# Kernel optimization log

Measured on AMD Instinct MI355X. Metric: run time of the kernel, lower is better.

## Reference

```python
import jax, jax.numpy as jnp
import numpy as np

N = 100000   # nodes
E = 1600000  # edges
D = 64       # input_size == hidden_size
L = 2        # n_layer


def setup_inputs() -> dict:
    key = jax.random.key(0)
    ks = jax.random.split(key, 16)
    s = 1.0 / np.sqrt(D)  # glorot-ish scale
    inp = jax.random.normal(ks[0], (N, D), jnp.float32)
    h = jax.random.normal(ks[1], (L, N, D), jnp.float32)
    edgidx = jax.random.randint(ks[2], (2, E), 0, N, jnp.int32)
    W = lambda i: jax.random.normal(ks[i], (L, D, D), jnp.float32) * s
    b = lambda i: jax.random.normal(ks[i], (L, D), jnp.float32) * 0.01
    return {
        'inp': inp, 'h': h, 'edgidx': edgidx,
        'Wxz': W(3), 'Whz': W(4), 'Wxr': W(5), 'Whr': W(6), 'Wxh': W(7), 'Whh': W(8),
        'bxz': b(9), 'bhz': b(10), 'bxr': b(11), 'bhr': b(12), 'bxh': b(13), 'bhh': b(14),
    }


def _gcn_norm(edgidx):
    # add self loops with weight 2 (improved=True), symmetric deg^-1/2 normalization
    row, col = edgidx[0], edgidx[1]
    loop = jnp.arange(N, dtype=row.dtype)
    row_f = jnp.concatenate([row, loop])
    col_f = jnp.concatenate([col, loop])
    w = jnp.concatenate([jnp.ones((E,), jnp.float32), 2.0 * jnp.ones((N,), jnp.float32)])
    deg = jax.ops.segment_sum(w, row_f, num_segments=N)
    dinv = jnp.where(deg > 0, deg ** -0.5, 0.0)
    norm = dinv[row_f] * w * dinv[col_f]
    return row_f, col_f, norm


def _gcn(x, Wt, bt, row_f, col_f, norm):
    # out[i] = sum_{(j->i)} norm_e * (x @ W)[j] + b   (PyG flow: gather at edge_index[0], scatter at edge_index[1])
    y = x @ Wt
    out = jax.ops.segment_sum(norm[:, None] * y[row_f], col_f, num_segments=N)
    return out + bt


def reference(inp, h, edgidx, Wxz, Whz, Wxr, Whr, Wxh, Whh, bxz, bhz, bxr, bhr, bxh, bhh):
    row_f, col_f, norm = _gcn_norm(edgidx)
    g = lambda x, W, b, i: _gcn(x, W[i], b[i], row_f, col_f, norm)
    x_in = inp
    outs = []
    for i in range(L):
        z = jax.nn.sigmoid(g(x_in, Wxz, bxz, i) + g(h[i], Whz, bhz, i))
        r = jax.nn.sigmoid(g(x_in, Wxr, bxr, i) + g(h[i], Whr, bhr, i))
        h_t = jnp.tanh(g(x_in, Wxh, bxh, i) + g(r * h[i], Whh, bhh, i))
        ho = z * h[i] + (1.0 - z) * h_t
        outs.append(ho)
        x_in = ho
    h_out = jnp.stack(outs)
    return (h_out, h_out)
```

## Files before the change

kernel.cpp:

```cpp
#include <hip/hip_runtime.h>
#include <hip/hip_fp16.h>
#include <math.h>
#include <stdint.h>

#define DD 64
#define CHUNK 1024
#define NRG 512
#define BB  128

using f16x8 = __attribute__((ext_vector_type(8))) _Float16;
using f32x4 = __attribute__((ext_vector_type(4))) float;

static inline int divup(int a, int b){ return (a + b - 1) / b; }

__global__ __launch_bounds__(256) void bin_k(
    const int* __restrict__ edg, int E, int per, int nr, int cap,
    unsigned int* __restrict__ bufc, unsigned short* __restrict__ bufr,
    int* __restrict__ cntc, int* __restrict__ cntr)
{
  extern __shared__ int cur[];
  int* curc = cur;
  int* curr = cur + nr;
  const int b = blockIdx.x, t = threadIdx.x;
  for (int i = t; i < 2 * nr; i += 256) cur[i] = 0;
  __syncthreads();
  const int e0 = b * per;
  const int e1 = (e0 + per < E) ? e0 + per : E;
  unsigned int* mybufc = bufc + (size_t)b * nr * cap;
  unsigned short* mybufr = bufr + (size_t)b * nr * cap;
  for (int e = e0 + t; e < e1; e += 256){
    int r = edg[e];
    int c = edg[E + e];
    int rg = c >> 9;
    int p = atomicAdd(&curc[rg], 1);
    if (p < cap) mybufc[rg * cap + p] = ((unsigned int)r << 9) | (unsigned int)(c & 511);
    int rr = r >> 9;
    int q = atomicAdd(&curr[rr], 1);
    if (q < cap) mybufr[rr * cap + q] = (unsigned short)(r & 511);
  }
  __syncthreads();
  for (int i = t; i < nr; i += 256){
    int vc = curc[i]; cntc[b * nr + i] = vc < cap ? vc : cap;
    int vr = curr[i]; cntr[b * nr + i] = vr < cap ? vr : cap;
  }
}

__global__ __launch_bounds__(256) void cnt2_k(
    const unsigned int* __restrict__ bufc, const unsigned short* __restrict__ bufr,
    const int* __restrict__ cntc, const int* __restrict__ cntr,
    int nb, int nr, int cap,
    int* __restrict__ colcnt, int* __restrict__ rowcnt, int N)
{
  __shared__ int lhc[NRG];
  __shared__ int lhr[NRG];
  __shared__ int lcc[BB];
  __shared__ int lcr[BB];
  const int rg = blockIdx.x, t = threadIdx.x;
  for (int i = t; i < NRG; i += 256){ lhc[i] = 0; lhr[i] = 0; }
  for (int i = t; i < nb; i += 256){ lcc[i] = cntc[i * nr + rg]; lcr[i] = cntr[i * nr + rg]; }
  __syncthreads();
  const int wv = t >> 6, lane = t & 63;
  for (int b = wv; b < nb; b += 4){
    const unsigned int* buf = bufc + ((size_t)b * nr + rg) * cap;
    int cnt = lcc[b];
    for (int i = lane; i < cnt; i += 64) atomicAdd(&lhc[buf[i] & 511], 1);
    const unsigned short* bufR = bufr + ((size_t)b * nr + rg) * cap;
    int cntR = lcr[b];
    for (int i = lane; i < cntR; i += 64) atomicAdd(&lhr[bufR[i]], 1);
  }
  __syncthreads();
  for (int i = t; i < NRG; i += 256){
    int node = rg * NRG + i;
    if (node < N){ colcnt[node] = lhc[i]; rowcnt[node] = lhr[i]; }
  }
}

__global__ void scan1_k(const int* __restrict__ cnt, const int* __restrict__ rowcnt,
                        float* __restrict__ dinv, int* __restrict__ bsum, int N){
  __shared__ int sh[256];
  int t = threadIdx.x;
  int base = blockIdx.x * CHUNK + t * 4;
  int s = 0;
  #pragma unroll
  for (int j = 0; j < 4; j++){
    int g = base + j;
    if (g < N){
      s += cnt[g];
      dinv[g] = 1.0f / sqrtf((float)rowcnt[g] + 2.0f);
    }
  }
  sh[t] = s; __syncthreads();
  for (int off = 128; off > 0; off >>= 1){
    if (t < off) sh[t] += sh[t + off];
    __syncthreads();
  }
  if (t == 0) bsum[blockIdx.x] = sh[0];
}

__global__ void scan2_k(const int* __restrict__ bsum, int* __restrict__ bpre, int NB){
  __shared__ int sh[128];
  int t = threadIdx.x;
  int v = (t < NB) ? bsum[t] : 0;
  sh[t] = v; __syncthreads();
  for (int off = 1; off < 128; off <<= 1){
    int x = (t >= off) ? sh[t - off] : 0;
    __syncthreads();
    sh[t] += x;
    __syncthreads();
  }
  if (t < NB) bpre[t] = sh[t] - v;
}

__global__ void scan3_k(const int* __restrict__ cnt, const int* __restrict__ bpre,
                        int* __restrict__ offsets, int N){
  __shared__ int sh[256];
  int t = threadIdx.x, b = blockIdx.x;
  int base = b * CHUNK + t * 4;
  int v[4]; int s = 0;
  #pragma unroll
  for (int j = 0; j < 4; j++){ int g = base + j; v[j] = (g < N) ? cnt[g] : 0; s += v[j]; }
  sh[t] = s; __syncthreads();
  for (int off = 1; off < 256; off <<= 1){
    int x = (t >= off) ? sh[t - off] : 0;
    __syncthreads();
    sh[t] += x;
    __syncthreads();
  }
  int run = sh[t] - s + bpre[b];
  #pragma unroll
  for (int j = 0; j < 4; j++){
    int g = base + j;
    if (g <= N) offsets[g] = run;
    run += v[j];
  }
}

__global__ __launch_bounds__(256) void scat_k(
    const unsigned int* __restrict__ bufc, const int* __restrict__ cntc,
    int nb, int nr, int cap, const int* __restrict__ offsets,
    const float* __restrict__ dinv,
    int* __restrict__ csr_src, float* __restrict__ csr_w, int N)
{
  __shared__ int loff[NRG];
  __shared__ float ldinv[NRG];
  __shared__ int lcc[BB];
  const int rg = blockIdx.x, t = threadIdx.x;
  for (int i = t; i < NRG; i += 256){
    int node = rg * NRG + i;
    loff[i]  = (node < N) ? offsets[node] : 0;
    ldinv[i] = (node < N) ? dinv[node] : 0.0f;
  }
  for (int i = t; i < nb; i += 256) lcc[i] = cntc[i * nr + rg];
  __syncthreads();
  const int wv = t >> 6, lane = t & 63;
  for (int b = wv; b < nb; b += 4){
    const unsigned int* buf = bufc + ((size_t)b * nr + rg) * cap;
    int cnt = lcc[b];
    for (int i = lane; i < cnt; i += 64){
      unsigned int v = buf[i];
      int lo = v & 511;
      int sn = (int)(v >> 9);
      int p = atomicAdd(&loff[lo], 1);
      csr_src[p] = sn;
      csr_w[p] = dinv[sn] * ldinv[lo];
    }
  }
}

__global__ void pack0_k(const float* __restrict__ X, const float* __restrict__ H,
                        __half2* __restrict__ XH, int total){
  int i = blockIdx.x * 256 + threadIdx.x;
  if (i < total){
    __half2 v;
    v.x = __float2half_rn(X[i]);
    v.y = __float2half_rn(H[i]);
    XH[i] = v;
  }
}

__global__ void packb_k(const float* __restrict__ Wxz, const float* __restrict__ Whz,
                        const float* __restrict__ Wxr, const float* __restrict__ Whr,
                        const float* __restrict__ Wxh, const float* __restrict__ Whh,
                        const float* __restrict__ bxz, const float* __restrict__ bhz,
                        const float* __restrict__ bxr, const float* __restrict__ bhr,
                        const float* __restrict__ bxh, const float* __restrict__ bhh,
                        _Float16* __restrict__ Bg, _Float16* __restrict__ Bo,
                        float* __restrict__ biasg, int L){
  const int PER = 24576 + 4096 + 192;
  int tid = blockIdx.x * 256 + threadIdx.x;
  if (tid >= L * PER) return;
  int l = tid / PER, r = tid % PER;
  if (r < 24576){
    int q = r;
    int s = q & 7, lane = (q >> 3) & 63, ks = (q >> 9) & 3, jt = q >> 11;
    int k = ks * 32 + (lane >> 4) * 8 + s;
    int b = jt >> 2;
    int j = (jt & 3) * 16 + (lane & 15);
    const float* Wx = (b == 0) ? Wxz : (b == 1) ? Wxr : Wxh;
    const float* Wh = (b == 0) ? Whz : Whr;
    float v;
    if (k < 64) v = Wx[(size_t)l * 4096 + k * 64 + j];
    else        v = (b == 2) ? 0.0f : Wh[(size_t)l * 4096 + (k - 64) * 64 + j];
    Bg[(size_t)l * 24576 + q] = (_Float16)v;
  } else if (r < 24576 + 4096){
    int q = r - 24576;
    int s = q & 7, lane = (q >> 3) & 63, ks = (q >> 9) & 1, jt = q >> 10;
    int k = ks * 32 + (lane >> 4) * 8 + s;
    int j = jt * 16 + (lane & 15);
    Bo[(size_t)l * 4096 + q] = (_Float16)Whh[(size_t)l * 4096 + k * 64 + j];
  } else {
    int j = r - (24576 + 4096);
    int b = j >> 6, jj = j & 63;
    float v = (b == 0) ? bxz[l * 64 + jj] + bhz[l * 64 + jj]
            : (b == 1) ? bxr[l * 64 + jj] + bhr[l * 64 + jj]
                       : bxh[l * 64 + jj] + bhh[l * 64 + jj];
    biasg[l * 192 + j] = v;
  }
}

__global__ void agg2_k(const __half2* __restrict__ XH,
                       const int* __restrict__ offsets, const int* __restrict__ src,
                       const float* __restrict__ w, const float* __restrict__ dinv,
                       _Float16* __restrict__ AXAH, int N){
  int wid = (blockIdx.x * blockDim.x + threadIdx.x) >> 6;
  int lane = threadIdx.x & 63;
  if (wid >= N) return;
  float dv = dinv[wid];
  float selfw = 2.0f * dv * dv;
  size_t me = (size_t)wid * DD + lane;
  float2 sf = __half22float2(XH[me]);
  float ax[8], ah[8];
  #pragma unroll
  for (int j = 0; j < 8; j++){ ax[j] = 0.0f; ah[j] = 0.0f; }
  ax[0] = selfw * sf.x; ah[0] = selfw * sf.y;
  int s0 = offsets[wid], s1 = offsets[wid + 1];
  int e = s0;
  for (; e + 8 <= s1; e += 8){
    int   sn[8];
    float wn[8];
    float2 f[8];
    #pragma unroll
    for (int j = 0; j < 8; j++){ sn[j] = src[e + j]; wn[j] = w[e + j]; }
    #pragma unroll
    for (int j = 0; j < 8; j++) f[j] = __half22float2(XH[(size_t)sn[j] * DD + lane]);
    #pragma unroll
    for (int j = 0; j < 8; j++){
      ax[j] += wn[j] * f[j].x;
      ah[j] += wn[j] * f[j].y;
    }
  }
  for (; e < s1; ++e){
    float wa = w[e];
    float2 fa = __half22float2(XH[(size_t)src[e] * DD + lane]);
    ax[0] += wa * fa.x;
    ah[0] += wa * fa.y;
  }
  float axs = ((ax[0] + ax[1]) + (ax[2] + ax[3])) + ((ax[4] + ax[5]) + (ax[6] + ax[7]));
  float ahs = ((ah[0] + ah[1]) + (ah[2] + ah[3])) + ((ah[4] + ah[5]) + (ah[6] + ah[7]));
  size_t o = (size_t)wid * 128 + lane;
  AXAH[o]      = (_Float16)axs;
  AXAH[o + 64] = (_Float16)ahs;
}

__global__ void agg1_k(const _Float16* __restrict__ RH,
                       const int* __restrict__ offsets, const int* __restrict__ src,
                       const float* __restrict__ w, const float* __restrict__ dinv,
                       _Float16* __restrict__ Arh, int N){
  int wid = (blockIdx.x * blockDim.x + threadIdx.x) >> 6;
  int lane = threadIdx.x & 63;
  if (wid >= N) return;
  float dv = dinv[wid];
  float selfw = 2.0f * dv * dv;
  size_t me = (size_t)wid * DD + lane;
  float ax[8];
  #pragma unroll
  for (int j = 0; j < 8; j++) ax[j] = 0.0f;
  ax[0] = selfw * (float)RH[me];
  int s0 = offsets[wid], s1 = offsets[wid + 1];
  int e = s0;
  for (; e + 8 <= s1; e += 8){
    int   sn[8];
    float wn[8];
    float f[8];
    #pragma unroll
    for (int j = 0; j < 8; j++){ sn[j] = src[e + j]; wn[j] = w[e + j]; }
    #pragma unroll
    for (int j = 0; j < 8; j++) f[j] = (float)RH[(size_t)sn[j] * DD + lane];
    #pragma unroll
    for (int j = 0; j < 8; j++) ax[j] += wn[j] * f[j];
  }
  for (; e < s1; ++e){
    ax[0] += w[e] * (float)RH[(size_t)src[e] * DD + lane];
  }
  Arh[me] = (_Float16)(((ax[0] + ax[1]) + (ax[2] + ax[3])) + ((ax[4] + ax[5]) + (ax[6] + ax[7])));
}

__global__ __launch_bounds__(256) void gatem_k(
    const _Float16* __restrict__ AXAH, const float* __restrict__ Hh,
    const _Float16* __restrict__ Bg, const float* __restrict__ biasg,
    _Float16* __restrict__ zb, _Float16* __restrict__ rhb,
    _Float16* __restrict__ t1b, int N)
{
  const int lane = threadIdx.x & 63;
  const int wv   = threadIdx.x >> 6;
  const long nbase = ((long)blockIdx.x * 4 + wv) * 32;
  if (nbase >= N) return;
  const int m  = lane & 15;
  const int kb = lane >> 4;

  f32x4 acc[2][12];
  #pragma unroll
  for (int jt = 0; jt < 12; jt++){
    float bv = biasg[jt * 16 + m];
    f32x4 b4 = {bv, bv, bv, bv};
    acc[0][jt] = b4;
    acc[1][jt] = b4;
  }

  #pragma unroll 1
  for (int ks = 0; ks < 4; ks++){
    f16x8 af0, af1;
    {
      long r0 = nbase + m;           if (r0 >= N) r0 = N - 1;
      long r1 = nbase + 16 + m;      if (r1 >= N) r1 = N - 1;
      af0 = *(const f16x8*)(AXAH + (size_t)r0 * 128 + ks * 32 + kb * 8);
      af1 = *(const f16x8*)(AXAH + (size_t)r1 * 128 + ks * 32 + kb * 8);
    }
    #pragma unroll
    for (int jt = 0; jt < 12; jt++){
      f16x8 bf = *(const f16x8*)(Bg + ((size_t)(jt * 4 + ks) * 64 + lane) * 8);
      acc[0][jt] = __builtin_amdgcn_mfma_f32_16x16x32_f16(af0, bf, acc[0][jt], 0, 0, 0);
      acc[1][jt] = __builtin_amdgcn_mfma_f32_16x16x32_f16(af1, bf, acc[1][jt], 0, 0, 0);
    }
  }

  #pragma unroll
  for (int mt = 0; mt < 2; mt++){
    #pragma unroll
    for (int i = 0; i < 4; i++){
      long row = nbase + mt * 16 + kb * 4 + i;
      if (row < N){
        #pragma unroll
        for (int jq = 0; jq < 4; jq++){
          int j = jq * 16 + m;
          size_t o = (size_t)row * 64 + j;
          float zpre = acc[mt][jq][i];
          float rpre = acc[mt][4 + jq][i];
          float t1v  = acc[mt][8 + jq][i];
          float hv = Hh[o];
          zb[o]  = (_Float16)(1.0f / (1.0f + __expf(-zpre)));
          rhb[o] = (_Float16)(hv / (1.0f + __expf(-rpre)));
          t1b[o] = (_Float16)t1v;
        }
      }
    }
  }
}

__global__ __launch_bounds__(256) void outm_k(
    const _Float16* __restrict__ Arh, const _Float16* __restrict__ t1b,
    const _Float16* __restrict__ zb, const float* __restrict__ Hh,
    const _Float16* __restrict__ Bo,
    float* __restrict__ o1, float* __restrict__ o2,
    const float* __restrict__ hNext, __half2* __restrict__ XHnext,
    int doPack, int N)
{
  const int lane = threadIdx.x & 63;
  const int wv   = threadIdx.x >> 6;
  const long nbase = ((long)blockIdx.x * 4 + wv) * 32;
  if (nbase >= N) return;
  const int m  = lane & 15;
  const int kb = lane >> 4;

  f32x4 acc[2][4];
  #pragma unroll
  for (int mt = 0; mt < 2; mt++){
    #pragma unroll
    for (int jt = 0; jt < 4; jt++){
      #pragma unroll
      for (int i = 0; i < 4; i++){
        long row = nbase + mt * 16 + kb * 4 + i;
        if (row >= N) row = N - 1;
        acc[mt][jt][i] = (float)t1b[(size_t)row * 64 + jt * 16 + m];
      }
    }
  }

  #pragma unroll
  for (int ks = 0; ks < 2; ks++){
    f16x8 af0, af1;
    {
      long r0 = nbase + m;           if (r0 >= N) r0 = N - 1;
      long r1 = nbase + 16 + m;      if (r1 >= N) r1 = N - 1;
      af0 = *(const f16x8*)(Arh + (size_t)r0 * 64 + ks * 32 + kb * 8);
      af1 = *(const f16x8*)(Arh + (size_t)r1 * 64 + ks * 32 + kb * 8);
    }
    #pragma unroll
    for (int jt = 0; jt < 4; jt++){
      f16x8 bf = *(const f16x8*)(Bo + ((size_t)(jt * 2 + ks) * 64 + lane) * 8);
      acc[0][jt] = __builtin_amdgcn_mfma_f32_16x16x32_f16(af0, bf, acc[0][jt], 0, 0, 0);
      acc[1][jt] = __builtin_amdgcn_mfma_f32_16x16x32_f16(af1, bf, acc[1][jt], 0, 0, 0);
    }
  }

  #pragma unroll
  for (int mt = 0; mt < 2; mt++){
    #pragma unroll
    for (int i = 0; i < 4; i++){
      long row = nbase + mt * 16 + kb * 4 + i;
      if (row < N){
        #pragma unroll
        for (int jt = 0; jt < 4; jt++){
          int j = jt * 16 + m;
          size_t o = (size_t)row * 64 + j;
          float e = __expf(2.0f * acc[mt][jt][i]);
          float ht = 1.0f - 2.0f / (e + 1.0f);
          float z = (float)zb[o];
          float hv = Hh[o];
          float ho = z * hv + (1.0f - z) * ht;
          o1[o] = ho;
          o2[o] = ho;
          if (doPack){
            __half2 v;
            v.x = __float2half_rn(ho);
            v.y = __float2half_rn(hNext[o]);
            XHnext[o] = v;
          }
        }
      }
    }
  }
}

extern "C" void kernel_launch(void* const* d_in, const int* in_sizes, int n_in,
                              void* d_out, int out_size, void* d_ws, size_t ws_size,
                              hipStream_t stream){
  const float* inp = (const float*)d_in[0];
  const float* h   = (const float*)d_in[1];
  const int*   edg = (const int*)d_in[2];
  const float* Wxz = (const float*)d_in[3];
  const float* Whz = (const float*)d_in[4];
  const float* Wxr = (const float*)d_in[5];
  const float* Whr = (const float*)d_in[6];
  const float* Wxh = (const float*)d_in[7];
  const float* Whh = (const float*)d_in[8];
  const float* bxz = (const float*)d_in[9];
  const float* bhz = (const float*)d_in[10];
  const float* bxr = (const float*)d_in[11];
  const float* bhr = (const float*)d_in[12];
  const float* bxh = (const float*)d_in[13];
  const float* bhh = (const float*)d_in[14];
  float* out = (float*)d_out;

  const int ND = in_sizes[0];
  const int N  = ND / DD;
  const int E  = in_sizes[2] / 2;
  const int L  = in_sizes[1] / ND;

  const int nr  = divup(N, NRG);
  const int per = divup(E, BB);
  const int cap = (per / nr) * 3 + 64;

  char* p = (char*)d_ws;
  auto alloc = [&](size_t bytes) -> void* {
    void* r = (void*)p;
    p += ((bytes + 255) / 256) * 256;
    return r;
  };
  auto a256 = [](size_t b) -> size_t { return ((b + 255) / 256) * 256; };

  int*      offsets = (int*)alloc((size_t)(N + 1) * 4);
  int*      bsum    = (int*)alloc(128 * 4);
  int*      bpre    = (int*)alloc(128 * 4);
  float*    dinv    = (float*)alloc((size_t)N * 4);
  int*      colcnt  = (int*)alloc((size_t)2 * N * 4);
  int*      rowcnt  = colcnt + N;
  int*      cntc    = (int*)alloc((size_t)BB * nr * 4);
  int*      cntr    = (int*)alloc((size_t)BB * nr * 4);
  int*      csr_src = (int*)alloc((size_t)E * 4);
  float*    csr_w   = (float*)alloc((size_t)E * 4);
  __half2*  XH      = (__half2*)alloc((size_t)ND * 4);
  _Float16* Bg      = (_Float16*)alloc((size_t)L * 24576 * 2);
  _Float16* Bo      = (_Float16*)alloc((size_t)L * 4096 * 2);
  float*    biasg   = (float*)alloc((size_t)L * 192 * 4);

  size_t bufc_b  = a256((size_t)BB * nr * cap * 4);
  size_t bufr_b  = a256((size_t)BB * nr * cap * 2);
  size_t axah_b  = a256((size_t)N * 128 * 2);
  size_t nd2_b   = a256((size_t)ND * 2);
  size_t ov_b    = axah_b + 4 * nd2_b;
  if (bufc_b + bufr_b > ov_b) ov_b = bufc_b + bufr_b;
  char* ov = (char*)alloc(ov_b);
  unsigned int*   bufc = (unsigned int*)ov;
  unsigned short* bufr = (unsigned short*)(ov + bufc_b);
  _Float16* AXAH = (_Float16*)ov;
  _Float16* Arh  = (_Float16*)(ov + axah_b);
  _Float16* zb   = (_Float16*)(ov + axah_b + nd2_b);
  _Float16* t1b  = (_Float16*)(ov + axah_b + 2 * nd2_b);
  _Float16* rhb  = (_Float16*)(ov + axah_b + 3 * nd2_b);

  bin_k<<<BB, 256, 2 * nr * 4, stream>>>(edg, E, per, nr, cap, bufc, bufr, cntc, cntr);
  cnt2_k<<<nr, 256, 0, stream>>>(bufc, bufr, cntc, cntr, BB, nr, cap, colcnt, rowcnt, N);
  const int NB = divup(N, CHUNK);
  scan1_k<<<NB, 256, 0, stream>>>(colcnt, rowcnt, dinv, bsum, N);
  scan2_k<<<1, 128, 0, stream>>>(bsum, bpre, NB);
  scan3_k<<<NB, 256, 0, stream>>>(colcnt, bpre, offsets, N);
  scat_k<<<nr, 256, 0, stream>>>(bufc, cntc, BB, nr, cap, offsets, dinv, csr_src, csr_w, N);

  pack0_k<<<divup(ND, 256), 256, 0, stream>>>(inp, h, XH, ND);
  {
    const int PER = 24576 + 4096 + 192;
    packb_k<<<divup(L * PER, 256), 256, 0, stream>>>(
        Wxz, Whz, Wxr, Whr, Wxh, Whh,
        bxz, bhz, bxr, bhr, bxh, bhh, Bg, Bo, biasg, L);
  }

  const int aggBlocks = divup(N, 4);
  const int mBlocks   = divup(N, 128);

  for (int l = 0; l < L; l++){
    const float* Hh = h + (size_t)l * ND;
    agg2_k<<<aggBlocks, 256, 0, stream>>>(XH, offsets, csr_src, csr_w, dinv, AXAH, N);
    gatem_k<<<mBlocks, 256, 0, stream>>>(AXAH, Hh,
        Bg + (size_t)l * 24576, biasg + (size_t)l * 192, zb, rhb, t1b, N);
    agg1_k<<<aggBlocks, 256, 0, stream>>>(rhb, offsets, csr_src, csr_w, dinv, Arh, N);
    const int doPack = (l + 1 < L);
    outm_k<<<mBlocks, 256, 0, stream>>>(Arh, t1b, zb, Hh,
        Bo + (size_t)l * 4096,
        out + (size_t)l * ND, out + (size_t)L * ND + (size_t)l * ND,
        h + (size_t)(l + 1 < L ? l + 1 : l) * ND, XH, doPack, N);
  }
}
```

Before: 546.3 us.

## Factor GCN norm into node-side dinv scaling and fold scans into count kernel

Drops the per-edge weight array by pre-scaling the gathered node features with the source node's dinv and multiplying the aggregated sum by the destination node's dinv. The aggregation kernels no longer load an edge weight, and the CSR build no longer computes or writes one. The three-kernel global scan is replaced by a per-region local scan inside the count kernel plus a single small region-base scan, with final offsets written during scatter. This removes several kernel launches and one E-sized float stream. In exchange, fp16 rounding now happens on the scaled values, which adds slight numerical risk.

After: 528.5 us. 1.03x faster.

```diff
diff --git a/kernel.cpp b/kernel.cpp
--- a/kernel.cpp
+++ b/kernel.cpp
@@ -4,7 +4,6 @@
 #include <stdint.h>
 
 #define DD 64
-#define CHUNK 1024
 #define NRG 512
 #define BB  128
 
@@ -45,16 +44,17 @@
   }
 }
 
-__global__ __launch_bounds__(256) void cnt2_k(
+__global__ __launch_bounds__(256) void cnt2b_k(
     const unsigned int* __restrict__ bufc, const unsigned short* __restrict__ bufr,
     const int* __restrict__ cntc, const int* __restrict__ cntr,
     int nb, int nr, int cap,
-    int* __restrict__ colcnt, int* __restrict__ rowcnt, int N)
+    int* __restrict__ locoff, int* __restrict__ rtot, float* __restrict__ dinv, int N)
 {
   __shared__ int lhc[NRG];
   __shared__ int lhr[NRG];
   __shared__ int lcc[BB];
   __shared__ int lcr[BB];
+  __shared__ int ps[256];
   const int rg = blockIdx.x, t = threadIdx.x;
   for (int i = t; i < NRG; i += 256){ lhc[i] = 0; lhr[i] = 0; }
   for (int i = t; i < nb; i += 256){ lcc[i] = cntc[i * nr + rg]; lcr[i] = cntr[i * nr + rg]; }
@@ -71,84 +71,57 @@
   __syncthreads();
   for (int i = t; i < NRG; i += 256){
     int node = rg * NRG + i;
-    if (node < N){ colcnt[node] = lhc[i]; rowcnt[node] = lhr[i]; }
-  }
-}
-
-__global__ void scan1_k(const int* __restrict__ cnt, const int* __restrict__ rowcnt,
-                        float* __restrict__ dinv, int* __restrict__ bsum, int N){
+    if (node < N) dinv[node] = rsqrtf((float)lhr[i] + 2.0f);
+  }
+  int v0 = lhc[2 * t], v1 = lhc[2 * t + 1];
+  int s = v0 + v1;
+  ps[t] = s; __syncthreads();
+  for (int off = 1; off < 256; off <<= 1){
+    int x = (t >= off) ? ps[t - off] : 0;
+    __syncthreads();
+    ps[t] += x;
+    __syncthreads();
+  }
+  int excl = ps[t] - s;
+  int n0 = rg * NRG + 2 * t;
+  if (n0 < N)     locoff[n0]     = excl;
+  if (n0 + 1 < N) locoff[n0 + 1] = excl + v0;
+  if (t == 255) rtot[rg] = ps[255];
+}
+
+__global__ void rscan_k(const int* __restrict__ rtot, int* __restrict__ rbase,
+                        int* __restrict__ offsets, int nr, int E, int N){
   __shared__ int sh[256];
   int t = threadIdx.x;
-  int base = blockIdx.x * CHUNK + t * 4;
-  int s = 0;
-  #pragma unroll
-  for (int j = 0; j < 4; j++){
-    int g = base + j;
-    if (g < N){
-      s += cnt[g];
-      dinv[g] = 1.0f / sqrtf((float)rowcnt[g] + 2.0f);
-    }
-  }
-  sh[t] = s; __syncthreads();
-  for (int off = 128; off > 0; off >>= 1){
-    if (t < off) sh[t] += sh[t + off];
-    __syncthreads();
-  }
-  if (t == 0) bsum[blockIdx.x] = sh[0];
-}
-
-__global__ void scan2_k(const int* __restrict__ bsum, int* __restrict__ bpre, int NB){
-  __shared__ int sh[128];
-  int t = threadIdx.x;
-  int v = (t < NB) ? bsum[t] : 0;
+  int v = (t < nr) ? rtot[t] : 0;
   sh[t] = v; __syncthreads();
-  for (int off = 1; off < 128; off <<= 1){
-    int x = (t >= off) ? sh[t - off] : 0;
-    __syncthreads();
-    sh[t] += x;
-    __syncthreads();
-  }
-  if (t < NB) bpre[t] = sh[t] - v;
-}
-
-__global__ void scan3_k(const int* __restrict__ cnt, const int* __restrict__ bpre,
-                        int* __restrict__ offsets, int N){
-  __shared__ int sh[256];
-  int t = threadIdx.x, b = blockIdx.x;
-  int base = b * CHUNK + t * 4;
-  int v[4]; int s = 0;
-  #pragma unroll
-  for (int j = 0; j < 4; j++){ int g = base + j; v[j] = (g < N) ? cnt[g] : 0; s += v[j]; }
-  sh[t] = s; __syncthreads();
   for (int off = 1; off < 256; off <<= 1){
     int x = (t >= off) ? sh[t - off] : 0;
     __syncthreads();
     sh[t] += x;
     __syncthreads();
   }
-  int run = sh[t] - s + bpre[b];
-  #pragma unroll
-  for (int j = 0; j < 4; j++){
-    int g = base + j;
-    if (g <= N) offsets[g] = run;
-    run += v[j];
-  }
+  if (t < nr) rbase[t] = sh[t] - v;
+  if (t == 0) offsets[N] = E;
 }
 
 __global__ __launch_bounds__(256) void scat_k(
     const unsigned int* __restrict__ bufc, const int* __restrict__ cntc,
-    int nb, int nr, int cap, const int* __restrict__ offsets,
-    const float* __restrict__ dinv,
-    int* __restrict__ csr_src, float* __restrict__ csr_w, int N)
+    int nb, int nr, int cap, const int* __restrict__ locoff,
+    const int* __restrict__ rbase,
+    int* __restrict__ offsets, int* __restrict__ csr_src, int N)
 {
   __shared__ int loff[NRG];
-  __shared__ float ldinv[NRG];
   __shared__ int lcc[BB];
   const int rg = blockIdx.x, t = threadIdx.x;
+  const int base = rbase[rg];
   for (int i = t; i < NRG; i += 256){
     int node = rg * NRG + i;
-    loff[i]  = (node < N) ? offsets[node] : 0;
-    ldinv[i] = (node < N) ? dinv[node] : 0.0f;
+    if (node < N){
+      int o = base + locoff[node];
+      loff[i] = o;
+      offsets[node] = o;
+    } else loff[i] = 0;
   }
   for (int i = t; i < nb; i += 256) lcc[i] = cntc[i * nr + rg];
   __syncthreads();
@@ -158,22 +131,20 @@
     int cnt = lcc[b];
     for (int i = lane; i < cnt; i += 64){
       unsigned int v = buf[i];
-      int lo = v & 511;
-      int sn = (int)(v >> 9);
-      int p = atomicAdd(&loff[lo], 1);
-      csr_src[p] = sn;
-      csr_w[p] = dinv[sn] * ldinv[lo];
+      int p = atomicAdd(&loff[v & 511], 1);
+      csr_src[p] = (int)(v >> 9);
     }
   }
 }
 
 __global__ void pack0_k(const float* __restrict__ X, const float* __restrict__ H,
-                        __half2* __restrict__ XH, int total){
+                        const float* __restrict__ dinv, __half2* __restrict__ XH, int total){
   int i = blockIdx.x * 256 + threadIdx.x;
   if (i < total){
+    float dv = dinv[i >> 6];
     __half2 v;
-    v.x = __float2half_rn(X[i]);
-    v.y = __float2half_rn(H[i]);
+    v.x = __float2half_rn(dv * X[i]);
+    v.y = __float2half_rn(dv * H[i]);
     XH[i] = v;
   }
 }
@@ -220,83 +191,79 @@
 
 __global__ void agg2_k(const __half2* __restrict__ XH,
                        const int* __restrict__ offsets, const int* __restrict__ src,
-                       const float* __restrict__ w, const float* __restrict__ dinv,
+                       const float* __restrict__ dinv,
                        _Float16* __restrict__ AXAH, int N){
   int wid = (blockIdx.x * blockDim.x + threadIdx.x) >> 6;
   int lane = threadIdx.x & 63;
   if (wid >= N) return;
   float dv = dinv[wid];
-  float selfw = 2.0f * dv * dv;
   size_t me = (size_t)wid * DD + lane;
   float2 sf = __half22float2(XH[me]);
   float ax[8], ah[8];
   #pragma unroll
   for (int j = 0; j < 8; j++){ ax[j] = 0.0f; ah[j] = 0.0f; }
-  ax[0] = selfw * sf.x; ah[0] = selfw * sf.y;
   int s0 = offsets[wid], s1 = offsets[wid + 1];
   int e = s0;
   for (; e + 8 <= s1; e += 8){
-    int   sn[8];
-    float wn[8];
+    int sn[8];
     float2 f[8];
     #pragma unroll
-    for (int j = 0; j < 8; j++){ sn[j] = src[e + j]; wn[j] = w[e + j]; }
+    for (int j = 0; j < 8; j++) sn[j] = src[e + j];
     #pragma unroll
     for (int j = 0; j < 8; j++) f[j] = __half22float2(XH[(size_t)sn[j] * DD + lane]);
     #pragma unroll
     for (int j = 0; j < 8; j++){
-      ax[j] += wn[j] * f[j].x;
-      ah[j] += wn[j] * f[j].y;
+      ax[j] += f[j].x;
+      ah[j] += f[j].y;
     }
   }
   for (; e < s1; ++e){
-    float wa = w[e];
     float2 fa = __half22float2(XH[(size_t)src[e] * DD + lane]);
-    ax[0] += wa * fa.x;
-    ah[0] += wa * fa.y;
+    ax[0] += fa.x;
+    ah[0] += fa.y;
   }
   float axs = ((ax[0] + ax[1]) + (ax[2] + ax[3])) + ((ax[4] + ax[5]) + (ax[6] + ax[7]));
   float ahs = ((ah[0] + ah[1]) + (ah[2] + ah[3])) + ((ah[4] + ah[5]) + (ah[6] + ah[7]));
   size_t o = (size_t)wid * 128 + lane;
-  AXAH[o]      = (_Float16)axs;
-  AXAH[o + 64] = (_Float16)ahs;
+  AXAH[o]      = (_Float16)(dv * (axs + 2.0f * sf.x));
+  AXAH[o + 64] = (_Float16)(dv * (ahs + 2.0f * sf.y));
 }
 
 __global__ void agg1_k(const _Float16* __restrict__ RH,
                        const int* __restrict__ offsets, const int* __restrict__ src,
-                       const float* __restrict__ w, const float* __restrict__ dinv,
+                       const float* __restrict__ dinv,
                        _Float16* __restrict__ Arh, int N){
   int wid = (blockIdx.x * blockDim.x + threadIdx.x) >> 6;
   int lane = threadIdx.x & 63;
   if (wid >= N) return;
   float dv = dinv[wid];
-  float selfw = 2.0f * dv * dv;
   size_t me = (size_t)wid * DD + lane;
+  float selfv = (float)RH[me];
   float ax[8];
   #pragma unroll
   for (int j = 0; j < 8; j++) ax[j] = 0.0f;
-  ax[0] = selfw * (float)RH[me];
   int s0 = offsets[wid], s1 = offsets[wid + 1];
   int e = s0;
   for (; e + 8 <= s1; e += 8){
-    int   sn[8];
-    float wn[8];
+    int sn[8];
     float f[8];
     #pragma unroll
-    for (int j = 0; j < 8; j++){ sn[j] = src[e + j]; wn[j] = w[e + j]; }
+    for (int j = 0; j < 8; j++) sn[j] = src[e + j];
     #pragma unroll
     for (int j = 0; j < 8; j++) f[j] = (float)RH[(size_t)sn[j] * DD + lane];
     #pragma unroll
-    for (int j = 0; j < 8; j++) ax[j] += wn[j] * f[j];
+    for (int j = 0; j < 8; j++) ax[j] += f[j];
   }
   for (; e < s1; ++e){
-    ax[0] += w[e] * (float)RH[(size_t)src[e] * DD + lane];
-  }
-  Arh[me] = (_Float16)(((ax[0] + ax[1]) + (ax[2] + ax[3])) + ((ax[4] + ax[5]) + (ax[6] + ax[7])));
+    ax[0] += (float)RH[(size_t)src[e] * DD + lane];
+  }
+  float axs = ((ax[0] + ax[1]) + (ax[2] + ax[3])) + ((ax[4] + ax[5]) + (ax[6] + ax[7]));
+  Arh[me] = (_Float16)(dv * (axs + 2.0f * selfv));
 }
 
 __global__ __launch_bounds__(256) void gatem_k(
     const _Float16* __restrict__ AXAH, const float* __restrict__ Hh,
+    const float* __restrict__ dinv,
     const _Float16* __restrict__ Bg, const float* __restrict__ biasg,
     _Float16* __restrict__ zb, _Float16* __restrict__ rhb,
     _Float16* __restrict__ t1b, int N)
@@ -340,6 +307,7 @@
     for (int i = 0; i < 4; i++){
       long row = nbase + mt * 16 + kb * 4 + i;
       if (row < N){
+        float dvr = dinv[row];
         #pragma unroll
         for (int jq = 0; jq < 4; jq++){
           int j = jq * 16 + m;
@@ -349,7 +317,7 @@
           float t1v  = acc[mt][8 + jq][i];
           float hv = Hh[o];
           zb[o]  = (_Float16)(1.0f / (1.0f + __expf(-zpre)));
-          rhb[o] = (_Float16)(hv / (1.0f + __expf(-rpre)));
+          rhb[o] = (_Float16)(dvr * hv / (1.0f + __expf(-rpre)));
           t1b[o] = (_Float16)t1v;
         }
       }
@@ -360,6 +328,7 @@
 __global__ __launch_bounds__(256) void outm_k(
     const _Float16* __restrict__ Arh, const _Float16* __restrict__ t1b,
     const _Float16* __restrict__ zb, const float* __restrict__ Hh,
+    const float* __restrict__ dinv,
     const _Float16* __restrict__ Bo,
     float* __restrict__ o1, float* __restrict__ o2,
     const float* __restrict__ hNext, __half2* __restrict__ XHnext,
@@ -409,6 +378,7 @@
     for (int i = 0; i < 4; i++){
       long row = nbase + mt * 16 + kb * 4 + i;
       if (row < N){
+        float dvr = dinv[row];
         #pragma unroll
         for (int jt = 0; jt < 4; jt++){
           int j = jt * 16 + m;
@@ -422,8 +392,8 @@
           o2[o] = ho;
           if (doPack){
             __half2 v;
-            v.x = __float2half_rn(ho);
-            v.y = __float2half_rn(hNext[o]);
+            v.x = __float2half_rn(dvr * ho);
+            v.y = __float2half_rn(dvr * hNext[o]);
             XHnext[o] = v;
           }
         }
@@ -470,15 +440,13 @@
   auto a256 = [](size_t b) -> size_t { return ((b + 255) / 256) * 256; };
 
   int*      offsets = (int*)alloc((size_t)(N + 1) * 4);
-  int*      bsum    = (int*)alloc(128 * 4);
-  int*      bpre    = (int*)alloc(128 * 4);
+  int*      locoff  = (int*)alloc((size_t)N * 4);
+  int*      rtot    = (int*)alloc(256 * 4);
+  int*      rbase   = (int*)alloc(256 * 4);
   float*    dinv    = (float*)alloc((size_t)N * 4);
-  int*      colcnt  = (int*)alloc((size_t)2 * N * 4);
-  int*      rowcnt  = colcnt + N;
   int*      cntc    = (int*)alloc((size_t)BB * nr * 4);
   int*      cntr    = (int*)alloc((size_t)BB * nr * 4);
   int*      csr_src = (int*)alloc((size_t)E * 4);
-  float*    csr_w   = (float*)alloc((size_t)E * 4);
   __half2*  XH      = (__half2*)alloc((size_t)ND * 4);
   _Float16* Bg      = (_Float16*)alloc((size_t)L * 24576 * 2);
   _Float16* Bo      = (_Float16*)alloc((size_t)L * 4096 * 2);
@@ -500,14 +468,13 @@
   _Float16* rhb  = (_Float16*)(ov + axah_b + 3 * nd2_b);
 
   bin_k<<<BB, 256, 2 * nr * 4, stream>>>(edg, E, per, nr, cap, bufc, bufr, cntc, cntr);
-  cnt2_k<<<nr, 256, 0, stream>>>(bufc, bufr, cntc, cntr, BB, nr, cap, colcnt, rowcnt, N);
-  const int NB = divup(N, CHUNK);
-  scan1_k<<<NB, 256, 0, stream>>>(colcnt, rowcnt, dinv, bsum, N);
-  scan2_k<<<1, 128, 0, stream>>>(bsum, bpre, NB);
-  scan3_k<<<NB, 256, 0, stream>>>(colcnt, bpre, offsets, N);
-  scat_k<<<nr, 256, 0, stream>>>(bufc, cntc, BB, nr, cap, offsets, dinv, csr_src, csr_w, N);
-
-  pack0_k<<<divup(ND, 256), 256, 0, stream>>>(inp, h, XH, ND);
+  cnt2b_k<<<nr, 256, 0, stream>>>(bufc, bufr, cntc, cntr, BB, nr, cap,
+                                  locoff, rtot, dinv, N);
+  rscan_k<<<1, 256, 0, stream>>>(rtot, rbase, offsets, nr, E, N);
+  scat_k<<<nr, 256, 0, stream>>>(bufc, cntc, BB, nr, cap, locoff, rbase,
+                                 offsets, csr_src, N);
+
+  pack0_k<<<divup(ND, 256), 256, 0, stream>>>(inp, h, dinv, XH, ND);
   {
     const int PER = 24576 + 4096 + 192;
     packb_k<<<divup(L * PER, 256), 256, 0, stream>>>(
@@ -520,12 +487,12 @@
 
   for (int l = 0; l < L; l++){
     const float* Hh = h + (size_t)l * ND;
-    agg2_k<<<aggBlocks, 256, 0, stream>>>(XH, offsets, csr_src, csr_w, dinv, AXAH, N);
-    gatem_k<<<mBlocks, 256, 0, stream>>>(AXAH, Hh,
+    agg2_k<<<aggBlocks, 256, 0, stream>>>(XH, offsets, csr_src, dinv, AXAH, N);
+    gatem_k<<<mBlocks, 256, 0, stream>>>(AXAH, Hh, dinv,
         Bg + (size_t)l * 24576, biasg + (size_t)l * 192, zb, rhb, t1b, N);
-    agg1_k<<<aggBlocks, 256, 0, stream>>>(rhb, offsets, csr_src, csr_w, dinv, Arh, N);
+    agg1_k<<<aggBlocks, 256, 0, stream>>>(rhb, offsets, csr_src, dinv, Arh, N);
     const int doPack = (l + 1 < L);
-    outm_k<<<mBlocks, 256, 0, stream>>>(Arh, t1b, zb, Hh,
+    outm_k<<<mBlocks, 256, 0, stream>>>(Arh, t1b, zb, Hh, dinv,
         Bo + (size_t)l * 4096,
         out + (size_t)l * ND, out + (size_t)L * ND + (size_t)l * ND,
         h + (size_t)(l + 1 < L ? l + 1 : l) * ND, XH, doPack, N);
```
